# Optimization experiments

Hardware: AMD Instinct MI355X
Metric: run time of the kernel (lower is better)

## Reference

```python
import jax, jax.numpy as jnp
import numpy as np

R = 7            # radius
STRIDE = 2       # downsample_factor
K_SIDE = 2 * R + 1   # 15 -> K = 225 neighbors


def setup_inputs() -> dict:
    key = jax.random.key(0)
    B, H, W = 8, 512, 512
    # integer segment labels in [0, 64), stored as float32
    segments = jax.random.randint(key, (B, 1, H, W), 0, 64).astype(jnp.float32)
    return {"segments": segments}


def _local_equality_adj(segments):
    # segments: [B, 1, H_full, W_full]
    seg = segments[..., ::STRIDE, ::STRIDE]          # [B, 1, H, W]
    B, _, H, W = seg.shape
    x = seg[:, 0]                                    # [B, H, W]
    # zero-pad borders by R (unfold-style neighborhood extraction)
    padded = jnp.pad(x, ((0, 0), (R, R), (R, R)))    # [B, H+2R, W+2R]
    offs = jnp.arange(K_SIDE)
    dy, dx = jnp.meshgrid(offs, offs, indexing="ij")
    dy = dy.reshape(-1)                              # [K]
    dx = dx.reshape(-1)                              # [K]

    def gather(dy_i, dx_i):
        return jax.lax.dynamic_slice(padded, (0, dy_i, dx_i), (B, H, W))

    neighbors = jax.vmap(gather)(dy, dx)             # [K, B, H, W]
    neighbors = jnp.transpose(neighbors, (1, 0, 2, 3))  # [B, K, H, W]
    # broadcast equality: center [B,1,H,W] vs neighbors [B,K,H,W]
    adj = (seg == neighbors).astype(jnp.float32)     # [B, K, H, W]
    return adj


def reference(segments):
    return _local_equality_adj(segments)
```

## Files before the change

kernel.cpp:

```cpp
#include <hip/hip_runtime.h>


#define RAD 7
#define KS 15
#define HW 256
#define IN_W 512
#define PLANE (HW * HW)
#define CH 8
#define SROWS (CH + 2 * RAD)
#define SPITCH 272
#define NPAIR (SPITCH / 2)
#define NTASK (SROWS * NPAIR)

typedef float vf4 __attribute__((ext_vector_type(4)));

__global__ __launch_bounds__(512) void adj_rowband(const float* __restrict__ in,
                                                   float* __restrict__ out) {
    __shared__ float smem[SROWS][SPITCH];

    const int band = blockIdx.x;
    const int b    = blockIdx.y;
    const int pg   = blockIdx.z;
    const int y0   = band * CH;
    const int p_begin = pg ? 113 : 0;
    const int p_end   = pg ? 225 : 113;

    const int tid = threadIdx.x;
    const float* inb = in + (size_t)b * (IN_W * IN_W);

    for (int i = tid; i < NTASK; i += 512) {
        const int r  = i / NPAIR;
        const int pr = i - r * NPAIR;
        const int g  = y0 - RAD + r;
        const int c0 = 2 * pr - 8;
        float v0 = 0.0f, v1 = 0.0f;
        if ((unsigned)g < (unsigned)HW && (unsigned)c0 < (unsigned)HW) {
            const vf4 q = *(const vf4*)(inb + (size_t)(2 * g) * IN_W + 2 * c0);
            v0 = q.x;
            v1 = q.z;
        }
        smem[r][2 * pr]     = v0;
        smem[r][2 * pr + 1] = v1;
    }
    __syncthreads();

    const int wv   = tid >> 6;
    const int lane = tid & 63;
    const int x    = lane * 4;

    const vf4 own = *(const vf4*)&smem[wv + RAD][8 + x];
    const float s0 = own.x, s1 = own.y, s2 = own.z, s3 = own.w;

    float* op = out + ((size_t)(b * (KS * KS) + p_begin)) * PLANE
                    + (size_t)(y0 + wv) * HW + x;

    for (int p = p_begin; p < p_end; ++p, op += PLANE) {
        const int dy = p / KS;
        const int dx = p - dy * KS;
        const float* nrow = &smem[wv + dy][0];
        const int d4 = (dx + 1) & ~3;
        const vf4 w0 = *(const vf4*)(nrow + x + d4);
        const vf4 w1 = *(const vf4*)(nrow + x + d4 + 4);
        vf4 r;
        switch ((dx + 1) & 3) {
        case 0:
            r.x = (s0 == w0.x) ? 1.f : 0.f; r.y = (s1 == w0.y) ? 1.f : 0.f;
            r.z = (s2 == w0.z) ? 1.f : 0.f; r.w = (s3 == w0.w) ? 1.f : 0.f;
            break;
        case 1:
            r.x = (s0 == w0.y) ? 1.f : 0.f; r.y = (s1 == w0.z) ? 1.f : 0.f;
            r.z = (s2 == w0.w) ? 1.f : 0.f; r.w = (s3 == w1.x) ? 1.f : 0.f;
            break;
        case 2:
            r.x = (s0 == w0.z) ? 1.f : 0.f; r.y = (s1 == w0.w) ? 1.f : 0.f;
            r.z = (s2 == w1.x) ? 1.f : 0.f; r.w = (s3 == w1.y) ? 1.f : 0.f;
            break;
        default:
            r.x = (s0 == w0.w) ? 1.f : 0.f; r.y = (s1 == w1.x) ? 1.f : 0.f;
            r.z = (s2 == w1.y) ? 1.f : 0.f; r.w = (s3 == w1.z) ? 1.f : 0.f;
            break;
        }
        __builtin_nontemporal_store(r, (vf4*)op);
    }
}

extern "C" void kernel_launch(void* const* d_in, const int* in_sizes, int n_in,
                              void* d_out, int out_size, void* d_ws, size_t ws_size,
                              hipStream_t stream) {
    const float* segments = (const float*)d_in[0];
    float* out = (float*)d_out;
    dim3 grid(32, 8, 2);
    dim3 block(512);
    adj_rowband<<<grid, block, 0, stream>>>(segments, out);
}
```

Baseline: 459.2 us.

## Launch cooperative convoy kernel with periodic grid syncs over all 225 planes

Each block now covers a whole batch and row band and writes all 225 neighbor planes, instead of splitting the planes across two blocks. The kernel is launched cooperatively and calls a grid-wide sync every 45 planes, plus a workgroup barrier after every plane, so all blocks write the same output planes at roughly the same time and the DRAM write stream stays localized. Nontemporal stores become plain stores. The grid shrinks to 256 blocks, which halves parallelism, and the added syncs and barriers cost time in exchange for the hoped-for write locality.

```diff
diff --git a/kernel.cpp b/kernel.cpp
--- a/kernel.cpp
+++ b/kernel.cpp
@@ -1,4 +1,7 @@
 #include <hip/hip_runtime.h>
+#include <hip/hip_cooperative_groups.h>
+
+namespace cg = cooperative_groups;
 
 
 #define RAD 7
@@ -11,31 +14,31 @@
 #define SPITCH 272
 #define NPAIR (SPITCH / 2)
 #define NTASK (SROWS * NPAIR)
+#define SYNC_K 45
 
 typedef float vf4 __attribute__((ext_vector_type(4)));
 
-__global__ __launch_bounds__(512) void adj_rowband(const float* __restrict__ in,
-                                                   float* __restrict__ out) {
+__global__ __launch_bounds__(512) void adj_convoy(const float* __restrict__ in,
+                                                  float* __restrict__ out,
+                                                  int use_gsync) {
     __shared__ float smem[SROWS][SPITCH];
 
-    const int band = blockIdx.x;
-    const int b    = blockIdx.y;
-    const int pg   = blockIdx.z;
+    const int g    = blockIdx.x;
+    const int b    = g >> 5;
+    const int band = g & 31;
     const int y0   = band * CH;
-    const int p_begin = pg ? 113 : 0;
-    const int p_end   = pg ? 225 : 113;
+    const int tid  = threadIdx.x;
 
-    const int tid = threadIdx.x;
     const float* inb = in + (size_t)b * (IN_W * IN_W);
 
     for (int i = tid; i < NTASK; i += 512) {
         const int r  = i / NPAIR;
         const int pr = i - r * NPAIR;
-        const int g  = y0 - RAD + r;
+        const int gy = y0 - RAD + r;
         const int c0 = 2 * pr - 8;
         float v0 = 0.0f, v1 = 0.0f;
-        if ((unsigned)g < (unsigned)HW && (unsigned)c0 < (unsigned)HW) {
-            const vf4 q = *(const vf4*)(inb + (size_t)(2 * g) * IN_W + 2 * c0);
+        if ((unsigned)gy < (unsigned)HW && (unsigned)c0 < (unsigned)HW) {
+            const vf4 q = *(const vf4*)(inb + (size_t)(2 * gy) * IN_W + 2 * c0);
             v0 = q.x;
             v1 = q.z;
         }
@@ -51,12 +54,11 @@
     const vf4 own = *(const vf4*)&smem[wv + RAD][8 + x];
     const float s0 = own.x, s1 = own.y, s2 = own.z, s3 = own.w;
 
-    float* op = out + ((size_t)(b * (KS * KS) + p_begin)) * PLANE
+    float* op = out + (size_t)b * (KS * KS) * (size_t)PLANE
                     + (size_t)(y0 + wv) * HW + x;
 
-    for (int p = p_begin; p < p_end; ++p, op += PLANE) {
-        const int dy = p / KS;
-        const int dx = p - dy * KS;
+    int dy = 0, dx = 0;
+    for (int p = 0; p < KS * KS; ++p, op += PLANE) {
         const float* nrow = &smem[wv + dy][0];
         const int d4 = (dx + 1) & ~3;
         const vf4 w0 = *(const vf4*)(nrow + x + d4);
@@ -80,7 +82,14 @@
             r.z = (s2 == w1.y) ? 1.f : 0.f; r.w = (s3 == w1.z) ? 1.f : 0.f;
             break;
         }
-        __builtin_nontemporal_store(r, (vf4*)op);
+        *(vf4*)op = r;
+
+        if (++dx == KS) { dx = 0; ++dy; }
+
+        __builtin_amdgcn_s_barrier();
+        if (use_gsync && (p % SYNC_K) == (SYNC_K - 1) && p != KS * KS - 1) {
+            cg::this_grid().sync();
+        }
     }
 }
 
@@ -89,7 +98,12 @@
                               hipStream_t stream) {
     const float* segments = (const float*)d_in[0];
     float* out = (float*)d_out;
-    dim3 grid(32, 8, 2);
-    dim3 block(512);
-    adj_rowband<<<grid, block, 0, stream>>>(segments, out);
+    int use_gsync = 1;
+    void* args[] = { (void*)&segments, (void*)&out, (void*)&use_gsync };
+    hipError_t e = hipLaunchCooperativeKernel((void*)adj_convoy,
+                                              dim3(256), dim3(512),
+                                              args, 0, stream);
+    if (e != hipSuccess) {
+        adj_convoy<<<dim3(256), dim3(512), 0, stream>>>(segments, out, 0);
+    }
 }
```

Result: slower. 585.2 us (+27.4%).

## Register-block neighbor window per dy row and split work by dy groups

Applied to the files above, without the earlier changes.

Each thread now loads a 20-float window of the neighbor row once per dy and produces all 15 dx outputs from registers through a fully unrolled loop. This removes the per-offset LDS loads and the runtime switch on alignment. The grid now splits the 15 dy rows across three z-blocks instead of two halves of the offset range. The output stores also change from nontemporal to regular stores, which may change cache behavior on this write-bound kernel.

```diff
diff --git a/kernel.cpp b/kernel.cpp
--- a/kernel.cpp
+++ b/kernel.cpp
@@ -14,28 +14,27 @@
 
 typedef float vf4 __attribute__((ext_vector_type(4)));
 
-__global__ __launch_bounds__(512) void adj_rowband(const float* __restrict__ in,
-                                                   float* __restrict__ out) {
+__global__ __launch_bounds__(512) void adj_regblock(const float* __restrict__ in,
+                                                    float* __restrict__ out) {
     __shared__ float smem[SROWS][SPITCH];
 
     const int band = blockIdx.x;
     const int b    = blockIdx.y;
-    const int pg   = blockIdx.z;
+    const int dyg  = blockIdx.z;
     const int y0   = band * CH;
-    const int p_begin = pg ? 113 : 0;
-    const int p_end   = pg ? 225 : 113;
+    const int dy0  = dyg * 5;
+    const int tid  = threadIdx.x;
 
-    const int tid = threadIdx.x;
     const float* inb = in + (size_t)b * (IN_W * IN_W);
 
     for (int i = tid; i < NTASK; i += 512) {
         const int r  = i / NPAIR;
         const int pr = i - r * NPAIR;
-        const int g  = y0 - RAD + r;
+        const int gy = y0 - RAD + r;
         const int c0 = 2 * pr - 8;
         float v0 = 0.0f, v1 = 0.0f;
-        if ((unsigned)g < (unsigned)HW && (unsigned)c0 < (unsigned)HW) {
-            const vf4 q = *(const vf4*)(inb + (size_t)(2 * g) * IN_W + 2 * c0);
+        if ((unsigned)gy < (unsigned)HW && (unsigned)c0 < (unsigned)HW) {
+            const vf4 q = *(const vf4*)(inb + (size_t)(2 * gy) * IN_W + 2 * c0);
             v0 = q.x;
             v1 = q.z;
         }
@@ -51,36 +50,32 @@
     const vf4 own = *(const vf4*)&smem[wv + RAD][8 + x];
     const float s0 = own.x, s1 = own.y, s2 = own.z, s3 = own.w;
 
-    float* op = out + ((size_t)(b * (KS * KS) + p_begin)) * PLANE
+    float* op = out + (size_t)b * (KS * KS) * (size_t)PLANE
+                    + (size_t)(dy0 * KS) * PLANE
                     + (size_t)(y0 + wv) * HW + x;
 
-    for (int p = p_begin; p < p_end; ++p, op += PLANE) {
-        const int dy = p / KS;
-        const int dx = p - dy * KS;
-        const float* nrow = &smem[wv + dy][0];
-        const int d4 = (dx + 1) & ~3;
-        const vf4 w0 = *(const vf4*)(nrow + x + d4);
-        const vf4 w1 = *(const vf4*)(nrow + x + d4 + 4);
-        vf4 r;
-        switch ((dx + 1) & 3) {
-        case 0:
-            r.x = (s0 == w0.x) ? 1.f : 0.f; r.y = (s1 == w0.y) ? 1.f : 0.f;
-            r.z = (s2 == w0.z) ? 1.f : 0.f; r.w = (s3 == w0.w) ? 1.f : 0.f;
-            break;
-        case 1:
-            r.x = (s0 == w0.y) ? 1.f : 0.f; r.y = (s1 == w0.z) ? 1.f : 0.f;
-            r.z = (s2 == w0.w) ? 1.f : 0.f; r.w = (s3 == w1.x) ? 1.f : 0.f;
-            break;
-        case 2:
-            r.x = (s0 == w0.z) ? 1.f : 0.f; r.y = (s1 == w0.w) ? 1.f : 0.f;
-            r.z = (s2 == w1.x) ? 1.f : 0.f; r.w = (s3 == w1.y) ? 1.f : 0.f;
-            break;
-        default:
-            r.x = (s0 == w0.w) ? 1.f : 0.f; r.y = (s1 == w1.x) ? 1.f : 0.f;
-            r.z = (s2 == w1.y) ? 1.f : 0.f; r.w = (s3 == w1.z) ? 1.f : 0.f;
-            break;
+    for (int dy = dy0; dy < dy0 + 5; ++dy) {
+        const float* wp = &smem[wv + dy][x];
+        const vf4 w0 = *(const vf4*)(wp);
+        const vf4 w1 = *(const vf4*)(wp + 4);
+        const vf4 w2 = *(const vf4*)(wp + 8);
+        const vf4 w3 = *(const vf4*)(wp + 12);
+        const vf4 w4 = *(const vf4*)(wp + 16);
+        const float win[20] = { w0.x, w0.y, w0.z, w0.w,
+                                w1.x, w1.y, w1.z, w1.w,
+                                w2.x, w2.y, w2.z, w2.w,
+                                w3.x, w3.y, w3.z, w3.w,
+                                w4.x, w4.y, w4.z, w4.w };
+        #pragma unroll
+        for (int dx = 0; dx < KS; ++dx) {
+            vf4 r;
+            r.x = (s0 == win[dx + 1]) ? 1.0f : 0.0f;
+            r.y = (s1 == win[dx + 2]) ? 1.0f : 0.0f;
+            r.z = (s2 == win[dx + 3]) ? 1.0f : 0.0f;
+            r.w = (s3 == win[dx + 4]) ? 1.0f : 0.0f;
+            *(vf4*)op = r;
+            op += PLANE;
         }
-        __builtin_nontemporal_store(r, (vf4*)op);
     }
 }
 
@@ -89,7 +84,7 @@
                               hipStream_t stream) {
     const float* segments = (const float*)d_in[0];
     float* out = (float*)d_out;
-    dim3 grid(32, 8, 2);
+    dim3 grid(32, 8, 3);
     dim3 block(512);
-    adj_rowband<<<grid, block, 0, stream>>>(segments, out);
+    adj_regblock<<<grid, block, 0, stream>>>(segments, out);
 }
```

Result: no change. 456.1 us (-0.7%).
